# Optimization experiments

Hardware: AMD Instinct MI355X
Metric: run time of the kernel (lower is better)

The kernel has to match this reference:

```python
import jax, jax.numpy as jnp
import numpy as np

N, E, DIM, NF, ED = 15000, 30000, 64, 3, 1

def _gru_cell(x, h, w_ih, w_hh, b_ih, b_hh):
    gi = x @ w_ih.T + b_ih
    gh = h @ w_hh.T + b_hh
    ir, iz, i_n = jnp.split(gi, 3, axis=-1)
    hr, hz, hn = jnp.split(gh, 3, axis=-1)
    r = jax.nn.sigmoid(ir + hr)
    z = jax.nn.sigmoid(iz + hz)
    n = jnp.tanh(i_n + r * hn)
    return (1.0 - z) * n + z * h

def _lstm_cell(x, h, c, w_ih, w_hh, b_ih, b_hh):
    g = x @ w_ih.T + b_ih + h @ w_hh.T + b_hh
    i, f, gg, o = jnp.split(g, 4, axis=-1)
    c2 = jax.nn.sigmoid(f) * c + jax.nn.sigmoid(i) * jnp.tanh(gg)
    return jax.nn.sigmoid(o) * jnp.tanh(c2), c2

def setup_inputs():
    key = jax.random.key(0)
    ks = jax.random.split(key, 32)
    p = lambda k, shape: jax.random.normal(k, shape, jnp.float32) * 0.05
    return {
        "x": jax.random.normal(ks[0], (N, NF), jnp.float32),
        "edge_index": jax.random.randint(ks[1], (2, E), 0, N),
        "edge_attr": jax.random.uniform(ks[2], (E, ED), jnp.float32),
        "lin0_w": p(ks[3], (DIM, NF)), "lin0_b": p(ks[4], (DIM,)),
        "e1_w": p(ks[5], (DIM, ED)), "e1_b": p(ks[6], (DIM,)),
        "e2_w": p(ks[7], (DIM * DIM, DIM)), "e2_b": p(ks[8], (DIM * DIM,)),
        "root_w": p(ks[9], (DIM, DIM)), "conv_b": p(ks[10], (DIM,)),
        "gru_w_ih": p(ks[11], (3 * DIM, DIM)), "gru_w_hh": p(ks[12], (3 * DIM, DIM)),
        "gru_b_ih": p(ks[13], (3 * DIM,)), "gru_b_hh": p(ks[14], (3 * DIM,)),
        "s2s_w_ih": p(ks[15], (4 * DIM, 2 * DIM)), "s2s_w_hh": p(ks[16], (4 * DIM, DIM)),
        "s2s_b_ih": p(ks[17], (4 * DIM,)), "s2s_b_hh": p(ks[18], (4 * DIM,)),
        "mem_w_ih": p(ks[19], (4 * DIM, 2 * DIM)), "mem_w_hh": p(ks[20], (4 * DIM, DIM)),
        "mem_b_ih": p(ks[21], (4 * DIM,)), "mem_b_hh": p(ks[22], (4 * DIM,)),
        "lin1_w": p(ks[23], (DIM, DIM)), "lin1_b": p(ks[24], (DIM,)),
        "lin3_w": p(ks[25], (1, DIM)), "lin3_b": p(ks[26], (1,)),
    }

def reference(x, edge_index, edge_attr, lin0_w, lin0_b, e1_w, e1_b, e2_w, e2_b,
              root_w, conv_b, gru_w_ih, gru_w_hh, gru_b_ih, gru_b_hh,
              s2s_w_ih, s2s_w_hh, s2s_b_ih, s2s_b_hh,
              mem_w_ih, mem_w_hh, mem_b_ih, mem_b_hh,
              lin1_w, lin1_b, lin3_w, lin3_b):
    n = x.shape[0]
    src, dst = edge_index[0], edge_index[1]
    # per-edge weight matrices from the edge MLP: [E, DIM, DIM] (edge_attr is constant across the 6 conv steps)
    he = jax.nn.relu(edge_attr @ e1_w.T + e1_b)
    We = (he @ e2_w.T + e2_b).reshape(-1, DIM, DIM)
    deg = jax.ops.segment_sum(jnp.ones(src.shape[0], jnp.float32), dst, num_segments=n)
    denom = jnp.maximum(deg, 1.0)[:, None]
    out = jax.nn.relu(x @ lin0_w.T + lin0_b)   # [N, DIM]
    h = out                                    # GRU hidden init = lin0 output
    for _ in range(6):
        msg = jnp.einsum('ei,eio->eo', out[src], We)          # gather + per-edge matmul
        agg = jax.ops.segment_sum(msg, dst, num_segments=n) / denom  # mean aggr
        m = jax.nn.relu(agg + out @ root_w + conv_b)          # NNConv root + bias
        h = _gru_cell(m, h, gru_w_ih, gru_w_hh, gru_b_ih, gru_b_hh)
        out = h
    # Set2Set pooling over a single graph (data.batch is all zeros)
    q_star = jnp.zeros((1, 2 * DIM), x.dtype)
    hs = jnp.zeros((1, DIM), x.dtype)
    cs = jnp.zeros((1, DIM), x.dtype)
    for _ in range(6):
        hs, cs = _lstm_cell(q_star, hs, cs, s2s_w_ih, s2s_w_hh, s2s_b_ih, s2s_b_hh)
        e = out @ hs[0]                     # [N] attention logits
        a = jax.nn.softmax(e)
        r = (a[:, None] * out).sum(0, keepdims=True)  # [1, DIM]
        q_star = jnp.concatenate([hs, r], axis=-1)     # [1, 2*DIM]
    hx, cx = _lstm_cell(q_star, jnp.zeros((1, DIM), x.dtype), jnp.zeros((1, DIM), x.dtype),
                        mem_w_ih, mem_w_hh, mem_b_ih, mem_b_hh)
    o = jax.nn.relu(hx @ lin1_w.T + lin1_b)
    v = o @ lin3_w.T + lin3_b               # [1, 1]
    return v, hx, cx
```

## Files before the change

### kernel.cpp

```cpp
#include <hip/hip_runtime.h>
#include <math.h>

#define Nn 15000
#define NP 15040
#define Ee 30000
#define NB_E 118
#define EB 938

#define OFF_AGG   0
#define OFF_DEG   962560
#define ZERO_END  977560
#define OFF_OUT   977568
#define OFF_DINV  1940128
#define OFF_AT    1955136
#define OFF_BT    2221376
#define OFF_PE    2496016
#define OFF_BH    2526016
#define OFF_SS    2541376
#define OFF_SD    2571376
#define OFF_SA    2601376
#define OFF_SP    2631376
#define OFF_PK    2661376
#define OFF_GMA   2690048
#define OFF_GSA   2690304
#define OFF_GRA   2690560
#define OFF_GMB   2706944
#define OFF_GSB   2707200
#define OFF_GRB   2707456
#define OFF_TSA   2723968
#define OFF_TSB   2740352
#define OFF_TMA   2756736
#define OFF_TMB   2773120
#define OFF_HSA   2789504
#define OFF_CSA   2789568
#define OFF_HSB   2789632
#define OFF_CSB   2789696
#define WS_FLOATS 2789760

#define SA_L0_END   3760
#define SA_WT2_END  3872
#define SA_WT3_END  4128
#define SA_Z_END    5083
#define SA_AB_END   6123
#define SA_EP_END   6241
#define ZERO_F4     244390

__device__ __forceinline__ float sigf(float x) { return 1.0f / (1.0f + expf(-x)); }
__device__ __forceinline__ float bcast(float v, int l) {
    return __int_as_float(__builtin_amdgcn_readlane(__float_as_int(v), l));
}
__device__ __forceinline__ int bcasti(int v, int l) {
    return __builtin_amdgcn_readlane(v, l);
}

__global__ __launch_bounds__(256) void k_setupAll(
        const float* __restrict__ x, const float* __restrict__ l0w,
        const float* __restrict__ l0b, float* __restrict__ out,
        const float* __restrict__ e1w, const float* __restrict__ e1b,
        const float* __restrict__ e2w, const float* __restrict__ e2b,
        float* __restrict__ At, float* __restrict__ Bt,
        const float* __restrict__ rootw, const float* __restrict__ whh,
        const float* __restrict__ wih, float* __restrict__ pk,
        const float* __restrict__ swih, const float* __restrict__ swhh,
        const float* __restrict__ mwih,
        float* __restrict__ tsa, float* __restrict__ tsb,
        float* __restrict__ tma, float* __restrict__ tmb,
        float* __restrict__ zbase,
        const int* __restrict__ ei, const float* __restrict__ ea,
        float* __restrict__ deg, int* __restrict__ pe, int* __restrict__ bh) {
    int b = blockIdx.x, tid = threadIdx.x;
    if (b < SA_L0_END) {
        int idx = b*256 + tid;
        int n = idx >> 6, o = idx & 63;
        float vv = 0.f;
        if (n < Nn)
            vv = fmaxf(l0b[o] + x[n*3+0]*l0w[o*3+0] + x[n*3+1]*l0w[o*3+1]
                       + x[n*3+2]*l0w[o*3+2], 0.f);
        out[idx] = vv;
    } else if (b < SA_WT2_END) {
        int idx = (b - SA_L0_END)*256 + tid;
        int g = idx >> 12;
        int t2 = idx & 4095;
        int q4 = t2 >> 2, k = t2 & 3;
        int lane = q4 & 63;
        int i4 = q4 >> 6;
        int i = i4*4 + k;
        float vv;
        if (g == 0)      vv = rootw[i*64 + lane];
        else if (g < 4)  vv = whh[((g-1)*64 + lane)*64 + i];
        else             vv = wih[((g-4)*64 + lane)*64 + i];
        pk[idx] = vv;
    } else if (b < SA_WT3_END) {
        int idx = (b - SA_WT2_END)*256 + tid;
        int t2 = idx >> 14, r = idx & 16383;
        int i = r >> 8, g = r & 255;
        if (t2 == 0)      tsa[r] = swih[g*128 + i] + swhh[g*64 + i];
        else if (t2 == 1) tsb[r] = swih[g*128 + 64 + i];
        else if (t2 == 2) tma[r] = mwih[g*128 + i];
        else              tmb[r] = mwih[g*128 + 64 + i];
    } else if (b < SA_Z_END) {
        int idx = (b - SA_WT3_END)*256 + tid;
        if (idx < ZERO_F4)
            ((float4*)zbase)[idx] = make_float4(0.f, 0.f, 0.f, 0.f);
    } else if (b < SA_AB_END) {
        __shared__ float t[64]; __shared__ int valid[64];
        __shared__ float sbp[65]; __shared__ int cnt;
        __shared__ float su[64], sv[64];
        int rel = b - SA_Z_END;
        int j = rel >> 4, qc = rel & 15;
        float w1 = 0.f, b1 = 0.f, tv = 0.f; int va = 0;
        if (tid < 64) {
            w1 = e1w[tid]; b1 = e1b[tid];
            if (w1 != 0.f) { tv = -b1 / w1; va = (tv > 0.f && tv < 1.f) ? 1 : 0; }
            t[tid] = tv; valid[tid] = va;
        }
        __syncthreads();
        if (tid < 64 && va) {
            int rank = 0;
            for (int kk = 0; kk < 64; ++kk)
                if (valid[kk] && (t[kk] < tv || (t[kk] == tv && kk < tid))) rank++;
            sbp[rank] = tv;
        }
        if (tid == 0) { int c = 0; for (int kk = 0; kk < 64; ++kk) c += valid[kk]; cnt = c; }
        __syncthreads();
        int m = cnt;
        if (j > m) return;
        if (tid < 64) {
            float lo = (j == 0) ? 0.f : sbp[j-1];
            float hi = (j == m) ? 1.f : sbp[j];
            float c = 0.5f * (lo + hi);
            int msk = (c * w1 + b1) > 0.f;
            su[tid] = msk ? w1 : 0.f;
            sv[tid] = msk ? b1 : 0.f;
        }
        __syncthreads();
        int q = qc*256 + tid;
        int i = q >> 6, o = q & 63;
        const float* row = e2w + q*64;
        float a = 0.f, bb = 0.f;
        #pragma unroll 8
        for (int k = 0; k < 64; ++k) { float w = row[k]; a = fmaf(su[k], w, a); bb = fmaf(sv[k], w, bb); }
        At[j*4096 + o*64 + i] = a;
        Bt[j*4096 + o*64 + i] = bb + e2b[q];
    } else {
        __shared__ float t[64]; __shared__ int valid[64];
        __shared__ float sbp[65]; __shared__ int cnt;
        __shared__ int lh[65];
        int eb = b - SA_AB_END;
        float w1 = 0.f, b1 = 0.f, tv = 0.f; int va = 0;
        if (tid < 64) {
            w1 = e1w[tid]; b1 = e1b[tid];
            if (w1 != 0.f) { tv = -b1 / w1; va = (tv > 0.f && tv < 1.f) ? 1 : 0; }
            t[tid] = tv; valid[tid] = va;
        }
        if (tid < 65) lh[tid] = 0;
        __syncthreads();
        if (tid < 64 && va) {
            int rank = 0;
            for (int kk = 0; kk < 64; ++kk)
                if (valid[kk] && (t[kk] < tv || (t[kk] == tv && kk < tid))) rank++;
            sbp[rank] = tv;
        }
        if (tid == 0) { int c = 0; for (int kk = 0; kk < 64; ++kk) c += valid[kk]; cnt = c; }
        __syncthreads();
        int m = cnt;
        int e = eb * 256 + tid;
        if (e < Ee) {
            atomicAdd(&deg[ei[Ee + e]], 1.0f);
            float a = ea[e];
            int p = 0;
            for (int jj = 0; jj < m; ++jj) p += (sbp[jj] <= a) ? 1 : 0;
            pe[e] = p;
            atomicAdd(&lh[p], 1);
        }
        __syncthreads();
        if (tid < 65) bh[eb*65 + tid] = lh[tid];
    }
}

__global__ __launch_bounds__(256) void k_scatter3(
        const float* __restrict__ deg, float* __restrict__ dinv,
        const int* __restrict__ ei, const float* __restrict__ ea,
        const int* __restrict__ pe, const int* __restrict__ bh,
        int* __restrict__ sS, int* __restrict__ sD,
        float* __restrict__ sA, int* __restrict__ sP) {
    int tid = threadIdx.x;
    if (blockIdx.x < 59) {
        int n = blockIdx.x * 256 + tid;
        if (n < Nn) dinv[n] = 1.0f / fmaxf(deg[n], 1.0f);
        return;
    }
    int eb = blockIdx.x - 59;
    __shared__ int stot[65], sown[65], sbase[65], cur[65];
    if (tid < 65) {
        int own = 0, tot = 0;
        for (int b2 = 0; b2 < NB_E; ++b2) {
            int v = bh[b2*65 + tid];
            if (b2 < eb) own += v;
            tot += v;
        }
        stot[tid] = tot; sown[tid] = own;
    }
    __syncthreads();
    if (tid == 0) {
        int run = 0;
        for (int j = 0; j < 65; ++j) { sbase[j] = run; run += stot[j]; }
    }
    __syncthreads();
    if (tid < 65) cur[tid] = sbase[tid] + sown[tid];
    __syncthreads();
    int e = eb * 256 + tid;
    if (e >= Ee) return;
    int p = pe[e];
    int pos = atomicAdd(&cur[p], 1);
    sS[pos] = ei[e]; sD[pos] = ei[Ee + e]; sA[pos] = ea[e]; sP[pos] = p;
}

__global__ __launch_bounds__(256) void k_edge4(
        const int* __restrict__ sS, const int* __restrict__ sD,
        const float* __restrict__ sA, const int* __restrict__ sP,
        const float* __restrict__ out, const float* __restrict__ At,
        const float* __restrict__ Bt, const float* __restrict__ dinv,
        float* __restrict__ agg) {
    int tid = threadIdx.x, lane = tid & 63;
    int wid = (blockIdx.x * 256 + tid) >> 6;
    const int CH = 8;
    int e0 = wid * CH;
    if (e0 >= Ee) return;
    int e1 = e0 + CH; if (e1 > Ee) e1 = Ee;
    int cnt = e1 - e0;

    int eidx = e0 + lane;
    int msrc = 0, mdst = 0, mp = 0; float ma = 0.f, mdv = 0.f;
    if (lane < cnt) {
        msrc = sS[eidx]; mdst = sD[eidx]; ma = sA[eidx]; mp = sP[eidx];
        mdv = dinv[mdst];
    }

    float Ar[64], Br[64];
    int curp = -1;
    float hv_next = out[bcasti(msrc, 0)*64 + lane];
    for (int j = 0; j < cnt; ++j) {
        float hv = hv_next;
        if (j+1 < cnt) hv_next = out[bcasti(msrc, j+1)*64 + lane];
        int p = bcasti(mp, j);
        if (p != curp) {
            curp = p;
            const float4* Ap4 = (const float4*)(At + p*4096 + lane*64);
            const float4* Bp4 = (const float4*)(Bt + p*4096 + lane*64);
            #pragma unroll
            for (int q = 0; q < 16; ++q) {
                float4 av = Ap4[q], bv = Bp4[q];
                Ar[q*4+0]=av.x; Ar[q*4+1]=av.y; Ar[q*4+2]=av.z; Ar[q*4+3]=av.w;
                Br[q*4+0]=bv.x; Br[q*4+1]=bv.y; Br[q*4+2]=bv.z; Br[q*4+3]=bv.w;
            }
        }
        float a = bcast(ma, j);
        float acc0 = 0.f, acc1 = 0.f;
        #pragma unroll
        for (int i = 0; i < 64; i += 2) {
            float h0 = bcast(hv, i);
            float h1 = bcast(hv, i+1);
            acc0 = fmaf(h0, fmaf(a, Ar[i],   Br[i]),   acc0);
            acc1 = fmaf(h1, fmaf(a, Ar[i+1], Br[i+1]), acc1);
        }
        float acc = (acc0 + acc1) * bcast(mdv, j);
        atomicAdd(&agg[bcasti(mdst, j)*64 + lane], acc);
    }
}

__global__ __launch_bounds__(512, 2) void k_gru9(
        float* __restrict__ out, float* __restrict__ agg,
        const float* __restrict__ pk, const float* __restrict__ convb,
        const float* __restrict__ gbih, const float* __restrict__ gbhh) {
    __shared__ __align__(16) float wL[7*4096];
    int tid = threadIdx.x, lane = tid & 63, w = tid >> 6;
    int n0 = blockIdx.x*64 + w*8;

    float hv[8], av[8];
    #pragma unroll
    for (int k = 0; k < 8; ++k) hv[k] = out[(n0+k)*64 + lane];
    #pragma unroll
    for (int k = 0; k < 8; ++k) {
        int gi = (n0+k)*64 + lane;
        av[k] = agg[gi];
        agg[gi] = 0.f;
    }

    {
        const float4* src = (const float4*)pk;
        float4* dst = (float4*)wL;
        #pragma unroll
        for (int i = 0; i < 14; ++i) dst[i*512 + tid] = src[i*512 + tid];
    }
    __syncthreads();
    const float4* wL4 = (const float4*)wL;

    float mv[8], ghr[8], ghz[8], ghn[8];
    float a0[8], a1[8], a2[8], a3[8];
    #pragma unroll
    for (int k = 0; k < 8; ++k) { a0[k]=0.f; a1[k]=0.f; a2[k]=0.f; a3[k]=0.f; }
    #pragma unroll 4
    for (int i4 = 0; i4 < 16; ++i4) {
        float4 w0 = wL4[(0*16+i4)*64 + lane];
        float4 w1 = wL4[(1*16+i4)*64 + lane];
        float4 w2 = wL4[(2*16+i4)*64 + lane];
        float4 w3 = wL4[(3*16+i4)*64 + lane];
        #pragma unroll
        for (int k = 0; k < 8; ++k) {
            float h;
            h = bcast(hv[k], i4*4+0);
            a0[k]=fmaf(h,w0.x,a0[k]); a1[k]=fmaf(h,w1.x,a1[k]);
            a2[k]=fmaf(h,w2.x,a2[k]); a3[k]=fmaf(h,w3.x,a3[k]);
            h = bcast(hv[k], i4*4+1);
            a0[k]=fmaf(h,w0.y,a0[k]); a1[k]=fmaf(h,w1.y,a1[k]);
            a2[k]=fmaf(h,w2.y,a2[k]); a3[k]=fmaf(h,w3.y,a3[k]);
            h = bcast(hv[k], i4*4+2);
            a0[k]=fmaf(h,w0.z,a0[k]); a1[k]=fmaf(h,w1.z,a1[k]);
            a2[k]=fmaf(h,w2.z,a2[k]); a3[k]=fmaf(h,w3.z,a3[k]);
            h = bcast(hv[k], i4*4+3);
            a0[k]=fmaf(h,w0.w,a0[k]); a1[k]=fmaf(h,w1.w,a1[k]);
            a2[k]=fmaf(h,w2.w,a2[k]); a3[k]=fmaf(h,w3.w,a3[k]);
        }
    }
    float cbv = convb[lane];
    #pragma unroll
    for (int k = 0; k < 8; ++k) {
        mv[k] = fmaxf(a0[k] + av[k] + cbv, 0.f);
        ghr[k] = a1[k]; ghz[k] = a2[k]; ghn[k] = a3[k];
    }

    #pragma unroll
    for (int k = 0; k < 8; ++k) { a0[k]=0.f; a1[k]=0.f; a2[k]=0.f; }
    #pragma unroll 4
    for (int i4 = 0; i4 < 16; ++i4) {
        float4 w4v = wL4[(4*16+i4)*64 + lane];
        float4 w5v = wL4[(5*16+i4)*64 + lane];
        float4 w6v = wL4[(6*16+i4)*64 + lane];
        #pragma unroll
        for (int k = 0; k < 8; ++k) {
            float h;
            h = bcast(mv[k], i4*4+0);
            a0[k]=fmaf(h,w4v.x,a0[k]); a1[k]=fmaf(h,w5v.x,a1[k]); a2[k]=fmaf(h,w6v.x,a2[k]);
            h = bcast(mv[k], i4*4+1);
            a0[k]=fmaf(h,w4v.y,a0[k]); a1[k]=fmaf(h,w5v.y,a1[k]); a2[k]=fmaf(h,w6v.y,a2[k]);
            h = bcast(mv[k], i4*4+2);
            a0[k]=fmaf(h,w4v.z,a0[k]); a1[k]=fmaf(h,w5v.z,a1[k]); a2[k]=fmaf(h,w6v.z,a2[k]);
            h = bcast(mv[k], i4*4+3);
            a0[k]=fmaf(h,w4v.w,a0[k]); a1[k]=fmaf(h,w5v.w,a1[k]); a2[k]=fmaf(h,w6v.w,a2[k]);
        }
    }

    float br  = gbih[lane]      + gbhh[lane];
    float bz  = gbih[64+lane]   + gbhh[64+lane];
    float bnI = gbih[128+lane];
    float bnH = gbhh[128+lane];
    #pragma unroll
    for (int k = 0; k < 8; ++k) {
        float r  = sigf(a0[k] + ghr[k] + br);
        float z  = sigf(a1[k] + ghz[k] + bz);
        float nn = tanhf(fmaf(r, ghn[k] + bnH, a2[k] + bnI));
        out[(n0+k)*64 + lane] = (1.f - z)*nn + z*hv[k];
    }
}

__global__ __launch_bounds__(512) void k_s2s(
        const float* __restrict__ tsa, const float* __restrict__ tsb,
        const float* __restrict__ bih, const float* __restrict__ bhh,
        const float* __restrict__ hs_rd, const float* __restrict__ cs_rd,
        float* __restrict__ hs_wr, float* __restrict__ cs_wr,
        const float* __restrict__ out,
        const float* __restrict__ gmax_rd, const float* __restrict__ gsum_rd,
        const float* __restrict__ gr_rd,
        float* __restrict__ gmax_wr, float* __restrict__ gsum_wr,
        float* __restrict__ gr_wr, int it) {
    __shared__ float red[512], shs[64], scs[64], srv[64], sg[256];
    __shared__ float wred[8], zred[8];
    __shared__ float sm_m[8], sm_z[8], sm_r[8][64];
    int tid = threadIdx.x, lane = tid & 63, w = tid >> 6;
    if (it == 0) {
        if (tid < 64) { shs[tid] = 0.f; scs[tid] = 0.f; srv[tid] = 0.f; }
        __syncthreads();
    } else {
        float gm = (tid < 256) ? gmax_rd[tid] : -3.4e38f;
        float wm = gm;
        #pragma unroll
        for (int off = 32; off > 0; off >>= 1) wm = fmaxf(wm, __shfl_xor(wm, off, 64));
        if (lane == 0) wred[w] = wm;
        __syncthreads();
        float M = fmaxf(fmaxf(fmaxf(wred[0], wred[1]), fmaxf(wred[2], wred[3])),
                        fmaxf(fmaxf(wred[4], wred[5]), fmaxf(wred[6], wred[7])));
        float zt = (tid < 256) ? gsum_rd[tid] * expf(gm - M) : 0.f;
        #pragma unroll
        for (int off = 32; off > 0; off >>= 1) zt += __shfl_xor(zt, off, 64);
        if (lane == 0) zred[w] = zt;
        float racc = 0.f;
        for (int b2 = w; b2 < 256; b2 += 8)
            racc = fmaf(gr_rd[b2*64 + lane], expf(gmax_rd[b2] - M), racc);
        red[tid] = racc;
        if (tid < 64) { shs[tid] = hs_rd[tid]; scs[tid] = cs_rd[tid]; }
        __syncthreads();
        if (w == 0) {
            float Z = zred[0]+zred[1]+zred[2]+zred[3]+zred[4]+zred[5]+zred[6]+zred[7];
            float s = 0.f;
            #pragma unroll
            for (int k = 0; k < 8; ++k) s += red[k*64 + lane];
            srv[lane] = s / Z;
        }
        __syncthreads();
    }
    if (tid < 256) {
        float g = bih[tid] + bhh[tid];
        #pragma unroll 8
        for (int i = 0; i < 64; ++i)
            g += shs[i]*tsa[i*256 + tid] + srv[i]*tsb[i*256 + tid];
        sg[tid] = g;
    }
    __syncthreads();
    if (tid < 64) {
        float ii = sigf(sg[tid]), ff = sigf(sg[64+tid]);
        float gg = tanhf(sg[128+tid]), oo = sigf(sg[192+tid]);
        float c2 = ff*scs[tid] + ii*gg;
        float hn = oo*tanhf(c2);
        shs[tid] = hn;
        if (blockIdx.x == 0) { hs_wr[tid] = hn; cs_wr[tid] = c2; }
    }
    __syncthreads();
    float hsv = shs[lane];
    float m = -3.4e38f, Z2 = 0.f, racc2 = 0.f;
    for (int n = blockIdx.x*8 + w; n < Nn; n += 2048) {
        float ov = out[n*64 + lane];
        float p = ov * hsv;
        #pragma unroll
        for (int off = 32; off > 0; off >>= 1) p += __shfl_xor(p, off, 64);
        float mn = fmaxf(m, p);
        float sc = expf(m - mn);
        float t  = expf(p - mn);
        Z2 = fmaf(Z2, sc, t);
        racc2 = fmaf(racc2, sc, t*ov);
        m = mn;
    }
    if (lane == 0) { sm_m[w] = m; sm_z[w] = Z2; }
    sm_r[w][lane] = racc2;
    __syncthreads();
    if (w == 0) {
        float M = sm_m[0];
        #pragma unroll
        for (int j = 1; j < 8; ++j) M = fmaxf(M, sm_m[j]);
        float Zb = 0.f, rb = 0.f;
        #pragma unroll
        for (int j = 0; j < 8; ++j) {
            float e = expf(sm_m[j] - M);
            Zb = fmaf(sm_z[j], e, Zb);
            rb = fmaf(sm_r[j][lane], e, rb);
        }
        gr_wr[blockIdx.x*64 + lane] = rb;
        if (lane == 0) { gmax_wr[blockIdx.x] = M; gsum_wr[blockIdx.x] = Zb; }
    }
}

__global__ __launch_bounds__(256) void k_final2(
        const float* __restrict__ tma, const float* __restrict__ tmb,
        const float* __restrict__ mbih, const float* __restrict__ mbhh,
        const float* __restrict__ hs,
        const float* __restrict__ gmax, const float* __restrict__ gsum,
        const float* __restrict__ gr,
        const float* __restrict__ l1w, const float* __restrict__ l1b,
        const float* __restrict__ l3w, const float* __restrict__ l3b,
        float* __restrict__ dout) {
    __shared__ float red[256], shs[64], srv[64], sg[256], shx[64], so[64];
    __shared__ float wred[4], zred[4];
    int tid = threadIdx.x, lane = tid & 63, w = tid >> 6;
    {
        float gm = gmax[tid];
        float wm = gm;
        #pragma unroll
        for (int off = 32; off > 0; off >>= 1) wm = fmaxf(wm, __shfl_xor(wm, off, 64));
        if (lane == 0) wred[w] = wm;
        __syncthreads();
        float M = fmaxf(fmaxf(wred[0], wred[1]), fmaxf(wred[2], wred[3]));
        float zt = gsum[tid] * expf(gm - M);
        #pragma unroll
        for (int off = 32; off > 0; off >>= 1) zt += __shfl_xor(zt, off, 64);
        if (lane == 0) zred[w] = zt;
        float racc = 0.f;
        for (int b2 = w; b2 < 256; b2 += 4)
            racc = fmaf(gr[b2*64 + lane], expf(gmax[b2] - M), racc);
        red[tid] = racc;
        if (tid < 64) shs[tid] = hs[tid];
        __syncthreads();
        if (w == 0) {
            float Z = zred[0]+zred[1]+zred[2]+zred[3];
            srv[lane] = (red[lane] + red[64+lane] + red[128+lane] + red[192+lane]) / Z;
        }
    }
    __syncthreads();
    {
        float g = mbih[tid] + mbhh[tid];
        #pragma unroll 8
        for (int i = 0; i < 64; ++i)
            g += shs[i]*tma[i*256 + tid] + srv[i]*tmb[i*256 + tid];
        sg[tid] = g;
    }
    __syncthreads();
    if (tid < 64) {
        float ii = sigf(sg[tid]);
        float gg = tanhf(sg[128+tid]);
        float oo = sigf(sg[192+tid]);
        float c2 = ii * gg;
        float hx = oo * tanhf(c2);
        shx[tid] = hx;
        dout[1 + tid] = hx;
        dout[65 + tid] = c2;
    }
    __syncthreads();
    if (tid < 64) {
        float a = l1b[tid];
        const float* wr = l1w + tid*64;
        #pragma unroll 8
        for (int i = 0; i < 64; ++i) a = fmaf(shx[i], wr[i], a);
        so[tid] = fmaxf(a, 0.f);
    }
    __syncthreads();
    if (tid == 0) {
        float v = l3b[0];
        for (int i = 0; i < 64; ++i) v = fmaf(so[i], l3w[i], v);
        dout[0] = v;
    }
}

extern "C" void kernel_launch(void* const* d_in, const int* in_sizes, int n_in,
                              void* d_out, int out_size, void* d_ws, size_t ws_size,
                              hipStream_t stream) {
    const float* x    = (const float*)d_in[0];
    const int*   ei   = (const int*)  d_in[1];
    const float* ea   = (const float*)d_in[2];
    const float* l0w  = (const float*)d_in[3];
    const float* l0b  = (const float*)d_in[4];
    const float* e1w  = (const float*)d_in[5];
    const float* e1b  = (const float*)d_in[6];
    const float* e2w  = (const float*)d_in[7];
    const float* e2b  = (const float*)d_in[8];
    const float* rootw= (const float*)d_in[9];
    const float* convb= (const float*)d_in[10];
    const float* gwih = (const float*)d_in[11];
    const float* gwhh = (const float*)d_in[12];
    const float* gbih = (const float*)d_in[13];
    const float* gbhh = (const float*)d_in[14];
    const float* swih = (const float*)d_in[15];
    const float* swhh = (const float*)d_in[16];
    const float* sbih = (const float*)d_in[17];
    const float* sbhh = (const float*)d_in[18];
    const float* mwih = (const float*)d_in[19];
    const float* mbih = (const float*)d_in[21];
    const float* mbhh = (const float*)d_in[22];
    const float* l1w  = (const float*)d_in[23];
    const float* l1b  = (const float*)d_in[24];
    const float* l3w  = (const float*)d_in[25];
    const float* l3b  = (const float*)d_in[26];

    float* ws   = (float*)d_ws;
    float* dout = (float*)d_out;
    if (ws_size < (size_t)WS_FLOATS * sizeof(float)) return;

    float* agg  = ws + OFF_AGG;
    float* deg  = ws + OFF_DEG;
    float* out  = ws + OFF_OUT;
    float* dinv = ws + OFF_DINV;
    float* At   = ws + OFF_AT;
    float* Bt   = ws + OFF_BT;
    int*   pe   = (int*)(ws + OFF_PE);
    int*   bh   = (int*)(ws + OFF_BH);
    int*   sS   = (int*)(ws + OFF_SS);
    int*   sD   = (int*)(ws + OFF_SD);
    float* sA   = ws + OFF_SA;
    int*   sP   = (int*)(ws + OFF_SP);
    float* pk   = ws + OFF_PK;
    float* gmA  = ws + OFF_GMA;
    float* gsA  = ws + OFF_GSA;
    float* grA  = ws + OFF_GRA;
    float* gmB  = ws + OFF_GMB;
    float* gsB  = ws + OFF_GSB;
    float* grB  = ws + OFF_GRB;
    float* tsa  = ws + OFF_TSA;
    float* tsb  = ws + OFF_TSB;
    float* tma  = ws + OFF_TMA;
    float* tmb  = ws + OFF_TMB;
    float* hsA  = ws + OFF_HSA;
    float* csA  = ws + OFF_CSA;
    float* hsB  = ws + OFF_HSB;
    float* csB  = ws + OFF_CSB;

    k_setupAll<<<SA_EP_END, 256, 0, stream>>>(x, l0w, l0b, out, e1w, e1b, e2w, e2b,
                                              At, Bt, rootw, gwhh, gwih, pk,
                                              swih, swhh, mwih, tsa, tsb, tma, tmb,
                                              ws + OFF_AGG, ei, ea, deg, pe, bh);
    k_scatter3<<<59 + NB_E, 256, 0, stream>>>(deg, dinv, ei, ea, pe, bh,
                                              sS, sD, sA, sP);

    for (int s = 0; s < 6; ++s) {
        k_edge4<<<EB, 256, 0, stream>>>(sS, sD, sA, sP, out, At, Bt, dinv, agg);
        k_gru9 <<<NP/64, 512, 0, stream>>>(out, agg, pk, convb, gbih, gbhh);
    }

    for (int it = 0; it < 6; ++it) {
        float* gm_rd = (it & 1) ? gmA : gmB;
        float* gs_rd = (it & 1) ? gsA : gsB;
        float* gr_rd = (it & 1) ? grA : grB;
        float* hs_rd = (it & 1) ? hsA : hsB;
        float* cs_rd = (it & 1) ? csA : csB;
        float* gm_wr = (it & 1) ? gmB : gmA;
        float* gs_wr = (it & 1) ? gsB : gsA;
        float* gr_wr = (it & 1) ? grB : grA;
        float* hs_wr = (it & 1) ? hsB : hsA;
        float* cs_wr = (it & 1) ? csB : csA;
        k_s2s<<<256, 512, 0, stream>>>(tsa, tsb, sbih, sbhh, hs_rd, cs_rd,
                                       hs_wr, cs_wr, out,
                                       gm_rd, gs_rd, gr_rd, gm_wr, gs_wr, gr_wr, it);
    }

    k_final2<<<1, 256, 0, stream>>>(tma, tmb, mbih, mbhh, hsB, gmB, gsB, grB,
                                    l1w, l1b, l3w, l3b, dout);
}
```

Baseline: 439.3 us.

## Replace atomic scatter aggregation with per-edge message buffer and destination gather lists

The edge kernel now writes each edge's message to a dense per-edge buffer instead of atomically adding into a per-node aggregate. A per-destination adjacency list (capped at MAXD=32 slots) is built once during setup, and the GRU kernel gathers and sums the incoming messages itself, scaling by the inverse degree. This removes float atomics and the per-step zeroing of the aggregate buffer. In exchange it writes and re-reads a large message buffer each step, and any node with more than 32 in-edges would overflow its list.

```diff
diff --git a/kernel.cpp b/kernel.cpp
--- a/kernel.cpp
+++ b/kernel.cpp
@@ -6,44 +6,45 @@
 #define Ee 30000
 #define NB_E 118
 #define EB 938
-
-#define OFF_AGG   0
-#define OFF_DEG   962560
-#define ZERO_END  977560
-#define OFF_OUT   977568
-#define OFF_DINV  1940128
-#define OFF_AT    1955136
-#define OFF_BT    2221376
-#define OFF_PE    2496016
-#define OFF_BH    2526016
-#define OFF_SS    2541376
-#define OFF_SD    2571376
-#define OFF_SA    2601376
-#define OFF_SP    2631376
-#define OFF_PK    2661376
-#define OFF_GMA   2690048
-#define OFF_GSA   2690304
-#define OFF_GRA   2690560
-#define OFF_GMB   2706944
-#define OFF_GSB   2707200
-#define OFF_GRB   2707456
-#define OFF_TSA   2723968
-#define OFF_TSB   2740352
-#define OFF_TMA   2756736
-#define OFF_TMB   2773120
-#define OFF_HSA   2789504
-#define OFF_CSA   2789568
-#define OFF_HSB   2789632
-#define OFF_CSB   2789696
-#define WS_FLOATS 2789760
+#define MAXD 32
+
+#define OFF_MSG   0
+#define OFF_DEG   1920000
+#define OFF_CNT   1935000
+#define ZERO_F4   7510
+#define OFF_OUT   1950040
+#define OFF_DINV  2912600
+#define OFF_AT    2927600
+#define OFF_BT    3193840
+#define OFF_PE    3460080
+#define OFF_BH    3490080
+#define OFF_SS    3497750
+#define OFF_SA    3527750
+#define OFF_SP    3557750
+#define OFF_DL    3587750
+#define OFF_PK    4069032
+#define OFF_GMA   4097704
+#define OFF_GSA   4097960
+#define OFF_GRA   4098216
+#define OFF_GMB   4114600
+#define OFF_GSB   4114856
+#define OFF_GRB   4115112
+#define OFF_TSA   4131496
+#define OFF_TSB   4147880
+#define OFF_TMA   4164264
+#define OFF_TMB   4180648
+#define OFF_HSA   4197032
+#define OFF_CSA   4197096
+#define OFF_HSB   4197160
+#define OFF_CSB   4197224
+#define WS_FLOATS 4197288
 
 #define SA_L0_END   3760
 #define SA_WT2_END  3872
 #define SA_WT3_END  4128
-#define SA_Z_END    5083
-#define SA_AB_END   6123
-#define SA_EP_END   6241
-#define ZERO_F4     244390
+#define SA_Z_END    4158
+#define SA_AB_END   5198
+#define SA_EP_END   5316
 
 __device__ __forceinline__ float sigf(float x) { return 1.0f / (1.0f + expf(-x)); }
 __device__ __forceinline__ float bcast(float v, int l) {
@@ -182,8 +183,8 @@
         const float* __restrict__ deg, float* __restrict__ dinv,
         const int* __restrict__ ei, const float* __restrict__ ea,
         const int* __restrict__ pe, const int* __restrict__ bh,
-        int* __restrict__ sS, int* __restrict__ sD,
-        float* __restrict__ sA, int* __restrict__ sP) {
+        int* __restrict__ sS, float* __restrict__ sA, int* __restrict__ sP,
+        int* __restrict__ cnt, int* __restrict__ dl) {
     int tid = threadIdx.x;
     if (blockIdx.x < 59) {
         int n = blockIdx.x * 256 + tid;
@@ -213,15 +214,17 @@
     if (e >= Ee) return;
     int p = pe[e];
     int pos = atomicAdd(&cur[p], 1);
-    sS[pos] = ei[e]; sD[pos] = ei[Ee + e]; sA[pos] = ea[e]; sP[pos] = p;
-}
-
-__global__ __launch_bounds__(256) void k_edge4(
-        const int* __restrict__ sS, const int* __restrict__ sD,
-        const float* __restrict__ sA, const int* __restrict__ sP,
-        const float* __restrict__ out, const float* __restrict__ At,
-        const float* __restrict__ Bt, const float* __restrict__ dinv,
-        float* __restrict__ agg) {
+    int dst = ei[Ee + e];
+    sS[pos] = ei[e]; sA[pos] = ea[e]; sP[pos] = p;
+    int slot = atomicAdd(&cnt[dst], 1);
+    dl[dst*MAXD + slot] = pos;
+}
+
+__global__ __launch_bounds__(256) void k_edge5(
+        const int* __restrict__ sS, const float* __restrict__ sA,
+        const int* __restrict__ sP, const float* __restrict__ out,
+        const float* __restrict__ At, const float* __restrict__ Bt,
+        float* __restrict__ msg) {
     int tid = threadIdx.x, lane = tid & 63;
     int wid = (blockIdx.x * 256 + tid) >> 6;
     const int CH = 8;
@@ -231,11 +234,8 @@
     int cnt = e1 - e0;
 
     int eidx = e0 + lane;
-    int msrc = 0, mdst = 0, mp = 0; float ma = 0.f, mdv = 0.f;
-    if (lane < cnt) {
-        msrc = sS[eidx]; mdst = sD[eidx]; ma = sA[eidx]; mp = sP[eidx];
-        mdv = dinv[mdst];
-    }
+    int msrc = 0, mp = 0; float ma = 0.f;
+    if (lane < cnt) { msrc = sS[eidx]; ma = sA[eidx]; mp = sP[eidx]; }
 
     float Ar[64], Br[64];
     int curp = -1;
@@ -264,13 +264,14 @@
             acc0 = fmaf(h0, fmaf(a, Ar[i],   Br[i]),   acc0);
             acc1 = fmaf(h1, fmaf(a, Ar[i+1], Br[i+1]), acc1);
         }
-        float acc = (acc0 + acc1) * bcast(mdv, j);
-        atomicAdd(&agg[bcasti(mdst, j)*64 + lane], acc);
-    }
-}
-
-__global__ __launch_bounds__(512, 2) void k_gru9(
-        float* __restrict__ out, float* __restrict__ agg,
+        msg[(e0 + j)*64 + lane] = acc0 + acc1;
+    }
+}
+
+__global__ __launch_bounds__(512, 2) void k_gru10(
+        float* __restrict__ out, const float* __restrict__ msg,
+        const int* __restrict__ cnt, const int* __restrict__ dl,
+        const float* __restrict__ dinv,
         const float* __restrict__ pk, const float* __restrict__ convb,
         const float* __restrict__ gbih, const float* __restrict__ gbhh) {
     __shared__ __align__(16) float wL[7*4096];
@@ -282,9 +283,13 @@
     for (int k = 0; k < 8; ++k) hv[k] = out[(n0+k)*64 + lane];
     #pragma unroll
     for (int k = 0; k < 8; ++k) {
-        int gi = (n0+k)*64 + lane;
-        av[k] = agg[gi];
-        agg[gi] = 0.f;
+        int n = n0 + k;
+        int cn = cnt[n];
+        const int* lst = dl + n*MAXD;
+        float s = 0.f;
+        for (int j = 0; j < cn; ++j)
+            s += msg[lst[j]*64 + lane];
+        av[k] = s * dinv[n];
     }
 
     {
@@ -563,8 +568,9 @@
     float* dout = (float*)d_out;
     if (ws_size < (size_t)WS_FLOATS * sizeof(float)) return;
 
-    float* agg  = ws + OFF_AGG;
+    float* msg  = ws + OFF_MSG;
     float* deg  = ws + OFF_DEG;
+    int*   cntp = (int*)(ws + OFF_CNT);
     float* out  = ws + OFF_OUT;
     float* dinv = ws + OFF_DINV;
     float* At   = ws + OFF_AT;
@@ -572,9 +578,9 @@
     int*   pe   = (int*)(ws + OFF_PE);
     int*   bh   = (int*)(ws + OFF_BH);
     int*   sS   = (int*)(ws + OFF_SS);
-    int*   sD   = (int*)(ws + OFF_SD);
     float* sA   = ws + OFF_SA;
     int*   sP   = (int*)(ws + OFF_SP);
+    int*   dl   = (int*)(ws + OFF_DL);
     float* pk   = ws + OFF_PK;
     float* gmA  = ws + OFF_GMA;
     float* gsA  = ws + OFF_GSA;
@@ -594,13 +600,14 @@
     k_setupAll<<<SA_EP_END, 256, 0, stream>>>(x, l0w, l0b, out, e1w, e1b, e2w, e2b,
                                               At, Bt, rootw, gwhh, gwih, pk,
                                               swih, swhh, mwih, tsa, tsb, tma, tmb,
-                                              ws + OFF_AGG, ei, ea, deg, pe, bh);
+                                              ws + OFF_DEG, ei, ea, deg, pe, bh);
     k_scatter3<<<59 + NB_E, 256, 0, stream>>>(deg, dinv, ei, ea, pe, bh,
-                                              sS, sD, sA, sP);
+                                              sS, sA, sP, cntp, dl);
 
     for (int s = 0; s < 6; ++s) {
-        k_edge4<<<EB, 256, 0, stream>>>(sS, sD, sA, sP, out, At, Bt, dinv, agg);
-        k_gru9 <<<NP/64, 512, 0, stream>>>(out, agg, pk, convb, gbih, gbhh);
+        k_edge5<<<EB, 256, 0, stream>>>(sS, sA, sP, out, At, Bt, msg);
+        k_gru10<<<NP/64, 512, 0, stream>>>(out, msg, cntp, dl, dinv,
+                                           pk, convb, gbih, gbhh);
     }
 
     for (int it = 0; it < 6; ++it) {
```

Result: slower. 499.4 us (+13.7%).
